# Optimization experiments

Hardware: AMD Instinct MI355X
Metric: run time of the kernel (lower is better)

## Reference

```python
import jax, jax.numpy as jnp
import numpy as np

H, D = 16, 64          # num_heads, head_dim
OUT = H * D            # out_dim = 1024
W1, W2 = 32, 32        # sliding windows
EPS_NORM = 1e-7
EPS_LN = 1e-5


def setup_inputs() -> dict:
    key = jax.random.key(0)
    ks = jax.random.split(key, 6)
    B, S, IN = 2, 2048, 1024
    x = jax.random.normal(ks[0], (B, S, IN), dtype=jnp.float32)
    scale = 0.02
    W_Q = jax.random.normal(ks[1], (IN, OUT), dtype=jnp.float32) * scale
    W_K = jax.random.normal(ks[2], (IN, OUT), dtype=jnp.float32) * scale
    W_V = jax.random.normal(ks[3], (IN, OUT), dtype=jnp.float32) * scale
    W_Kp = jax.random.normal(ks[4], (IN, OUT), dtype=jnp.float32) * scale
    W_O = jax.random.normal(ks[5], (OUT, OUT), dtype=jnp.float32) * scale
    ln_gamma = jnp.ones((OUT,), dtype=jnp.float32)
    ln_beta = jnp.zeros((OUT,), dtype=jnp.float32)
    return {"x": x, "W_Q": W_Q, "W_K": W_K, "W_V": W_V, "W_Kp": W_Kp,
            "W_O": W_O, "ln_gamma": ln_gamma, "ln_beta": ln_beta}


def _l2norm(t):
    return t / (jnp.linalg.norm(t, axis=-1, keepdims=True) + EPS_NORM)


def reference(x, W_Q, W_K, W_V, W_Kp, W_O, ln_gamma, ln_beta):
    B, S, _ = x.shape
    # projections -> (B, S, H, D)
    Q = _l2norm((x @ W_Q).reshape(B, S, H, D))
    K = _l2norm((x @ W_K).reshape(B, S, H, D))
    Kp = _l2norm((x @ W_Kp).reshape(B, S, H, D))
    V = (x @ W_V).reshape(B, S, H, D)
    # windowed keys/values (last w1/w2 positions, as in the PyTorch fallback)
    K_win = K[:, -W1:]
    Kp_win = Kp[:, -W2:]
    V_win = V[:, -W1:]
    Vp_win = V[:, -W2:]
    # triple product A_ijk = q.k.k' / sqrt(D) -> (B, S, H, w1, w2)
    A = jnp.einsum('bshd,bjhd,bkhd->bshjk', Q, K_win, Kp_win) / jnp.sqrt(jnp.float32(D))
    # causal window mask: allow j <= i + w1 - S and k <= i + w2 - S
    s_idx = jnp.arange(S)[:, None, None]
    j_idx = jnp.arange(W1)[None, :, None]
    k_idx = jnp.arange(W2)[None, None, :]
    mask = (j_idx > s_idx + (W1 - S)) | (k_idx > s_idx + (W2 - S))  # (S, w1, w2)
    neg_inf = jnp.float32(-jnp.inf)
    A = jnp.where(mask[None, :, None, :, :], neg_inf, A)
    # joint softmax over (j, k); fully-masked query rows produce zeros
    A_flat = A.reshape(B, S, H, W1 * W2)
    all_masked = jnp.all(A_flat == neg_inf, axis=-1, keepdims=True)
    A_safe = jnp.where(all_masked, 0.0, A_flat)
    P = jax.nn.softmax(A_safe, axis=-1)
    P = jnp.where(all_masked, 0.0, P).reshape(B, S, H, W1, W2)
    # value outer-product weighting (V' = V)
    Z = jnp.einsum('bshjk,bjhd,bkhd->bshd', P, V_win, Vp_win)
    out = Z.reshape(B, S, OUT) @ W_O
    out = out + x  # residual (shapes match)
    # LayerNorm
    mu = jnp.mean(out, axis=-1, keepdims=True)
    var = jnp.mean((out - mu) ** 2, axis=-1, keepdims=True)
    out = (out - mu) / jnp.sqrt(var + EPS_LN) * ln_gamma + ln_beta
    return out
```

## Files before the change

kernel.cpp:

```cpp
#include <hip/hip_runtime.h>
#include <math.h>


#define XS 68

#define YQ_OFF    0
#define YK_OFF    65536
#define YKP_OFF   131072
#define YV_OFF    196608
#define Z_OFF     262144
#define DELTA_OFF 327680
#define WS_FLOATS 393216

__global__ __launch_bounds__(256) void zero_ws(float4* __restrict__ ws) {
  ws[blockIdx.x * 256 + threadIdx.x] = make_float4(0.f, 0.f, 0.f, 0.f);
}

__global__ __launch_bounds__(256, 4) void proj_kernel(
    const float* __restrict__ x,
    const float* __restrict__ Wq, const float* __restrict__ Wk,
    const float* __restrict__ Wkp, const float* __restrict__ Wv,
    float* __restrict__ Y) {
  __shared__ float xs[64 * 65];
  const int tid = threadIdx.x;
  const int z    = blockIdx.x >> 4;
  const int col0 = (blockIdx.x & 15) * 64;
  const int k0   = blockIdx.y * 64;
  const float* __restrict__ W =
      (z == 0) ? Wq : ((z == 1) ? Wk : ((z == 2) ? Wkp : Wv));

  #pragma unroll
  for (int i = 0; i < 4; i++) {
    int e = i * 256 + tid;
    int r = e >> 4, q = e & 15;
    int b = r >> 5, t = r & 31;
    float4 v = *(const float4*)(x + ((b * 2048 + 2016 + t) * 1024 + k0 + q * 4));
    xs[(q * 4 + 0) * 65 + r] = v.x;
    xs[(q * 4 + 1) * 65 + r] = v.y;
    xs[(q * 4 + 2) * 65 + r] = v.z;
    xs[(q * 4 + 3) * 65 + r] = v.w;
  }
  __syncthreads();

  const int wave = __builtin_amdgcn_readfirstlane(tid >> 6);
  const int lane = tid & 63;
  const float* __restrict__ Wt = W + (size_t)k0 * 1024 + col0 + wave * 16;

  float acc[16];
  #pragma unroll
  for (int c = 0; c < 16; c++) acc[c] = 0.f;

  #pragma unroll 4
  for (int kk = 0; kk < 64; kk++) {
    float xv = xs[kk * 65 + lane];
    const float* __restrict__ wrow = Wt + kk * 1024;
    #pragma unroll
    for (int c = 0; c < 16; c++) acc[c] = fmaf(xv, wrow[c], acc[c]);
  }

  __syncthreads();
  #pragma unroll
  for (int c = 0; c < 16; c++) xs[lane * 65 + wave * 16 + c] = acc[c];
  __syncthreads();
  float* __restrict__ Yo = Y + z * 65536 + col0;
  #pragma unroll
  for (int i = 0; i < 16; i++) {
    int r = wave * 16 + i;
    atomicAdd(Yo + r * 1024 + lane, xs[r * 65 + lane]);
  }
}

__global__ __launch_bounds__(256) void attn_kernel(
    const float* __restrict__ Y, float* __restrict__ Zout) {
  __shared__ float Kn[32 * XS], Kp[32 * XS], Vs[32 * XS];
  __shared__ float Pt[4][32 * 33];
  __shared__ float qs[4][64];
  const int tid = threadIdx.x;
  const int wave = tid >> 6, lane = tid & 63;
  const int h = blockIdx.y, b = blockIdx.z;

  #pragma unroll
  for (int i = 0; i < 8; i++) {
    int e = i * 256 + tid;
    int row = e >> 6, d = e & 63;
    int src = (b * 32 + row) * 1024 + h * 64 + d;
    Kn[row * XS + d] = Y[YK_OFF + src];
    Kp[row * XS + d] = Y[YKP_OFF + src];
    Vs[row * XS + d] = Y[YV_OFF + src];
  }
  __syncthreads();

  for (int rr = 0; rr < 8; rr++) {
    int row = wave * 8 + rr;
    float kv = Kn[row * XS + lane];
    float s2 = kv * kv;
    #pragma unroll
    for (int off = 1; off < 64; off <<= 1) s2 += __shfl_xor(s2, off);
    Kn[row * XS + lane] = kv * (1.f / (sqrtf(s2) + 1e-7f));
    float pv = Kp[row * XS + lane];
    float p2 = pv * pv;
    #pragma unroll
    for (int off = 1; off < 64; off <<= 1) p2 += __shfl_xor(p2, off);
    Kp[row * XS + lane] = pv * (1.f / (sqrtf(p2) + 1e-7f));
  }
  __syncthreads();

  const int m = blockIdx.x * 4 + wave;
  const int r = b * 32 + m;

  float q = Y[YQ_OFF + r * 1024 + h * 64 + lane];
  float q2 = q * q;
  #pragma unroll
  for (int off = 1; off < 64; off <<= 1) q2 += __shfl_xor(q2, off);
  q *= (1.f / (sqrtf(q2) + 1e-7f));
  qs[wave][lane] = q;
  __builtin_amdgcn_wave_barrier();

  const int lj = lane >> 3, lk = lane & 7;
  float acc[4][4];
  #pragma unroll
  for (int a = 0; a < 4; a++)
    #pragma unroll
    for (int c = 0; c < 4; c++) acc[a][c] = 0.f;

  const float* qw = qs[wave];
  for (int dq = 0; dq < 16; dq++) {
    float4 q4 = *(const float4*)(qw + dq * 4);
    float4 t4[4], kp4[4];
    #pragma unroll
    for (int tj = 0; tj < 4; tj++) {
      float4 kv = *(const float4*)(Kn + (lj * 4 + tj) * XS + dq * 4);
      t4[tj].x = q4.x * kv.x; t4[tj].y = q4.y * kv.y;
      t4[tj].z = q4.z * kv.z; t4[tj].w = q4.w * kv.w;
    }
    #pragma unroll
    for (int tk = 0; tk < 4; tk++)
      kp4[tk] = *(const float4*)(Kp + (lk * 4 + tk) * XS + dq * 4);
    #pragma unroll
    for (int tj = 0; tj < 4; tj++)
      #pragma unroll
      for (int tk = 0; tk < 4; tk++)
        acc[tj][tk] += t4[tj].x * kp4[tk].x + t4[tj].y * kp4[tk].y
                     + t4[tj].z * kp4[tk].z + t4[tj].w * kp4[tk].w;
  }

  float amax = -1e30f;
  #pragma unroll
  for (int tj = 0; tj < 4; tj++)
    #pragma unroll
    for (int tk = 0; tk < 4; tk++) {
      int j = lj * 4 + tj, k = lk * 4 + tk;
      if (j <= m && k <= m) amax = fmaxf(amax, acc[tj][tk] * 0.125f);
    }
  #pragma unroll
  for (int off = 1; off < 64; off <<= 1) amax = fmaxf(amax, __shfl_xor(amax, off));

  float lsum = 0.f;
  float* ptw = Pt[wave];
  #pragma unroll
  for (int tj = 0; tj < 4; tj++)
    #pragma unroll
    for (int tk = 0; tk < 4; tk++) {
      int j = lj * 4 + tj, k = lk * 4 + tk;
      float e = 0.f;
      if (j <= m && k <= m) e = __expf(acc[tj][tk] * 0.125f - amax);
      lsum += e;
      ptw[k * 33 + j] = e;
    }
  #pragma unroll
  for (int off = 1; off < 64; off <<= 1) lsum += __shfl_xor(lsum, off);
  float inv = 1.f / lsum;
  __builtin_amdgcn_wave_barrier();

  float vreg[32];
  #pragma unroll
  for (int k = 0; k < 32; k++) vreg[k] = Vs[k * XS + lane];
  float zacc = 0.f;
  for (int k = 0; k <= m; k++) {
    float g = 0.f;
    #pragma unroll
    for (int j = 0; j < 32; j++) g += ptw[k * 33 + j] * vreg[j];
    zacc += g * vreg[k];
  }
  Zout[r * 1024 + h * 64 + lane] = zacc * inv;
}

__global__ __launch_bounds__(256, 4) void wo_kernel(
    const float* __restrict__ Zr, const float* __restrict__ Wo,
    float* __restrict__ delta) {
  __shared__ float xs[64 * 65];
  const int tid = threadIdx.x;
  const int col0 = blockIdx.x * 64;
  const int k0   = blockIdx.y * 32;

  #pragma unroll
  for (int i = 0; i < 2; i++) {
    int e = i * 256 + tid;
    int r = e >> 3, q = e & 7;
    float4 v = *(const float4*)(Zr + r * 1024 + k0 + q * 4);
    xs[(q * 4 + 0) * 65 + r] = v.x;
    xs[(q * 4 + 1) * 65 + r] = v.y;
    xs[(q * 4 + 2) * 65 + r] = v.z;
    xs[(q * 4 + 3) * 65 + r] = v.w;
  }
  __syncthreads();

  const int wave = __builtin_amdgcn_readfirstlane(tid >> 6);
  const int lane = tid & 63;
  const float* __restrict__ Wt = Wo + (size_t)k0 * 1024 + col0 + wave * 16;

  float acc[16];
  #pragma unroll
  for (int c = 0; c < 16; c++) acc[c] = 0.f;

  #pragma unroll 4
  for (int kk = 0; kk < 32; kk++) {
    float xv = xs[kk * 65 + lane];
    const float* __restrict__ wrow = Wt + kk * 1024;
    #pragma unroll
    for (int c = 0; c < 16; c++) acc[c] = fmaf(xv, wrow[c], acc[c]);
  }

  __syncthreads();
  #pragma unroll
  for (int c = 0; c < 16; c++) xs[lane * 65 + wave * 16 + c] = acc[c];
  __syncthreads();
  #pragma unroll
  for (int i = 0; i < 16; i++) {
    int r = wave * 16 + i;
    atomicAdd(delta + r * 1024 + col0 + lane, xs[r * 65 + lane]);
  }
}

__global__ __launch_bounds__(256, 4) void ln_kernel(
    const float4* __restrict__ x4, const float4* __restrict__ delta4,
    const float4* __restrict__ g4, const float4* __restrict__ b4,
    float4* __restrict__ out4) {
  const int tid = threadIdx.x;
  const int wave = tid >> 6, lane = tid & 63;
  const int row = blockIdx.x * 4 + wave;
  const int b = row >> 11, s = row & 2047;

  float4 v[4];
  #pragma unroll
  for (int i = 0; i < 4; i++) v[i] = x4[row * 256 + i * 64 + lane];
  if (s >= 2016) {
    int drow = b * 32 + (s - 2016);
    #pragma unroll
    for (int i = 0; i < 4; i++) {
      float4 d = delta4[drow * 256 + i * 64 + lane];
      v[i].x += d.x; v[i].y += d.y; v[i].z += d.z; v[i].w += d.w;
    }
  }
  float sum = 0.f, ss = 0.f;
  #pragma unroll
  for (int i = 0; i < 4; i++) {
    sum += v[i].x + v[i].y + v[i].z + v[i].w;
    ss  += v[i].x * v[i].x + v[i].y * v[i].y + v[i].z * v[i].z + v[i].w * v[i].w;
  }
  #pragma unroll
  for (int off = 1; off < 64; off <<= 1) {
    sum += __shfl_xor(sum, off);
    ss  += __shfl_xor(ss, off);
  }
  float mu   = sum * (1.f / 1024.f);
  float var  = ss * (1.f / 1024.f) - mu * mu;
  float rstd = rsqrtf(var + 1e-5f);

  #pragma unroll
  for (int i = 0; i < 4; i++) {
    float4 g = g4[i * 64 + lane];
    float4 be = b4[i * 64 + lane];
    float4 o;
    o.x = (v[i].x - mu) * rstd * g.x + be.x;
    o.y = (v[i].y - mu) * rstd * g.y + be.y;
    o.z = (v[i].z - mu) * rstd * g.z + be.z;
    o.w = (v[i].w - mu) * rstd * g.w + be.w;
    out4[row * 256 + i * 64 + lane] = o;
  }
}

extern "C" void kernel_launch(void* const* d_in, const int* in_sizes, int n_in,
                              void* d_out, int out_size, void* d_ws, size_t ws_size,
                              hipStream_t stream) {
  const float* x   = (const float*)d_in[0];
  const float* Wq  = (const float*)d_in[1];
  const float* Wk  = (const float*)d_in[2];
  const float* Wv  = (const float*)d_in[3];
  const float* Wkp = (const float*)d_in[4];
  const float* Wo  = (const float*)d_in[5];
  const float* gam = (const float*)d_in[6];
  const float* bet = (const float*)d_in[7];
  float* out = (float*)d_out;
  float* ws  = (float*)d_ws;

  hipLaunchKernelGGL(zero_ws, dim3(WS_FLOATS / 1024), dim3(256), 0, stream,
                     (float4*)ws);
  hipLaunchKernelGGL(proj_kernel, dim3(64, 16), dim3(256), 0, stream,
                     x, Wq, Wk, Wkp, Wv, ws);
  hipLaunchKernelGGL(attn_kernel, dim3(8, 16, 2), dim3(256), 0, stream,
                     ws, ws + Z_OFF);
  hipLaunchKernelGGL(wo_kernel, dim3(16, 32), dim3(256), 0, stream,
                     ws + Z_OFF, Wo, ws + DELTA_OFF);
  hipLaunchKernelGGL(ln_kernel, dim3(1024), dim3(256), 0, stream,
                     (const float4*)x, (const float4*)(ws + DELTA_OFF),
                     (const float4*)gam, (const float4*)bet, (float4*)out);
}
```

Before: 141.9 us.

## Replace atomic split-K accumulation with per-split partial buffers reduced by consumers

The projection and output-projection GEMMs now write split-K partials to separate workspace slices with plain stores instead of atomicAdd. The attention and LayerNorm kernels sum the partials when they read them, which removes the workspace-zeroing kernel and the atomic traffic. The K split changes from 64/32 to 128 with fewer blocks. Attention also gets a swizzled shared-memory layout for K and Kp and vectorised float4 P stores and loads. The cost is extra partial reads in the consumer kernels, fewer blocks in the GEMMs, and lower occupancy from the larger shared tile.

```diff
diff --git a/kernel.cpp b/kernel.cpp
--- a/kernel.cpp
+++ b/kernel.cpp
@@ -4,35 +4,34 @@
 
 #define XS 68
 
-#define YQ_OFF    0
-#define YK_OFF    65536
-#define YKP_OFF   131072
-#define YV_OFF    196608
-#define Z_OFF     262144
-#define DELTA_OFF 327680
-#define WS_FLOATS 393216
-
-__global__ __launch_bounds__(256) void zero_ws(float4* __restrict__ ws) {
-  ws[blockIdx.x * 256 + threadIdx.x] = make_float4(0.f, 0.f, 0.f, 0.f);
-}
-
-__global__ __launch_bounds__(256, 4) void proj_kernel(
+#define NSPLIT    8
+#define YPART_SZ  262144
+#define Z_OFF     (NSPLIT * YPART_SZ)
+#define DPART_OFF (Z_OFF + 65536)
+
+
+__device__ __forceinline__ int sw_idx(int row, int d) {
+  return row * 64 + ((((d >> 2) + (row >> 2)) & 15) << 2) + (d & 3);
+}
+
+__global__ __launch_bounds__(256, 2) void proj_kernel(
     const float* __restrict__ x,
     const float* __restrict__ Wq, const float* __restrict__ Wk,
     const float* __restrict__ Wkp, const float* __restrict__ Wv,
-    float* __restrict__ Y) {
-  __shared__ float xs[64 * 65];
+    float* __restrict__ ws) {
+  __shared__ float xs[128 * 65];
   const int tid = threadIdx.x;
   const int z    = blockIdx.x >> 4;
   const int col0 = (blockIdx.x & 15) * 64;
-  const int k0   = blockIdx.y * 64;
+  const int ks   = blockIdx.y;
+  const int k0   = ks * 128;
   const float* __restrict__ W =
       (z == 0) ? Wq : ((z == 1) ? Wk : ((z == 2) ? Wkp : Wv));
 
   #pragma unroll
-  for (int i = 0; i < 4; i++) {
+  for (int i = 0; i < 8; i++) {
     int e = i * 256 + tid;
-    int r = e >> 4, q = e & 15;
+    int r = e >> 5, q = e & 31;
     int b = r >> 5, t = r & 31;
     float4 v = *(const float4*)(x + ((b * 2048 + 2016 + t) * 1024 + k0 + q * 4));
     xs[(q * 4 + 0) * 65 + r] = v.x;
@@ -51,7 +50,7 @@
   for (int c = 0; c < 16; c++) acc[c] = 0.f;
 
   #pragma unroll 4
-  for (int kk = 0; kk < 64; kk++) {
+  for (int kk = 0; kk < 128; kk++) {
     float xv = xs[kk * 65 + lane];
     const float* __restrict__ wrow = Wt + kk * 1024;
     #pragma unroll
@@ -62,18 +61,19 @@
   #pragma unroll
   for (int c = 0; c < 16; c++) xs[lane * 65 + wave * 16 + c] = acc[c];
   __syncthreads();
-  float* __restrict__ Yo = Y + z * 65536 + col0;
+  float* __restrict__ Yo = ws + (size_t)ks * YPART_SZ + z * 65536 + col0;
   #pragma unroll
   for (int i = 0; i < 16; i++) {
     int r = wave * 16 + i;
-    atomicAdd(Yo + r * 1024 + lane, xs[r * 65 + lane]);
+    Yo[r * 1024 + lane] = xs[r * 65 + lane];
   }
 }
 
 __global__ __launch_bounds__(256) void attn_kernel(
-    const float* __restrict__ Y, float* __restrict__ Zout) {
-  __shared__ float Kn[32 * XS], Kp[32 * XS], Vs[32 * XS];
-  __shared__ float Pt[4][32 * 33];
+    const float* __restrict__ ws, float* __restrict__ Zout) {
+  __shared__ float Kn[32 * 64], Kp[32 * 64];
+  __shared__ float Vs[32 * XS];
+  __shared__ float Pt[4][32 * 36];
   __shared__ float qs[4][64];
   const int tid = threadIdx.x;
   const int wave = tid >> 6, lane = tid & 63;
@@ -84,31 +84,45 @@
     int e = i * 256 + tid;
     int row = e >> 6, d = e & 63;
     int src = (b * 32 + row) * 1024 + h * 64 + d;
-    Kn[row * XS + d] = Y[YK_OFF + src];
-    Kp[row * XS + d] = Y[YKP_OFF + src];
-    Vs[row * XS + d] = Y[YV_OFF + src];
+    float kn = 0.f, kp = 0.f, vv = 0.f;
+    #pragma unroll
+    for (int s = 0; s < NSPLIT; s++) {
+      const float* __restrict__ p = ws + (size_t)s * YPART_SZ + src;
+      kn += p[65536];
+      kp += p[131072];
+      vv += p[196608];
+    }
+    Kn[sw_idx(row, d)] = kn;
+    Kp[sw_idx(row, d)] = kp;
+    Vs[row * XS + d] = vv;
   }
   __syncthreads();
 
   for (int rr = 0; rr < 8; rr++) {
     int row = wave * 8 + rr;
-    float kv = Kn[row * XS + lane];
+    int a = sw_idx(row, lane);
+    float kv = Kn[a];
     float s2 = kv * kv;
     #pragma unroll
     for (int off = 1; off < 64; off <<= 1) s2 += __shfl_xor(s2, off);
-    Kn[row * XS + lane] = kv * (1.f / (sqrtf(s2) + 1e-7f));
-    float pv = Kp[row * XS + lane];
+    Kn[a] = kv * (1.f / (sqrtf(s2) + 1e-7f));
+    float pv = Kp[a];
     float p2 = pv * pv;
     #pragma unroll
     for (int off = 1; off < 64; off <<= 1) p2 += __shfl_xor(p2, off);
-    Kp[row * XS + lane] = pv * (1.f / (sqrtf(p2) + 1e-7f));
+    Kp[a] = pv * (1.f / (sqrtf(p2) + 1e-7f));
   }
   __syncthreads();
 
   const int m = blockIdx.x * 4 + wave;
   const int r = b * 32 + m;
 
-  float q = Y[YQ_OFF + r * 1024 + h * 64 + lane];
+  float q = 0.f;
+  {
+    int src = r * 1024 + h * 64 + lane;
+    #pragma unroll
+    for (int s = 0; s < NSPLIT; s++) q += ws[(size_t)s * YPART_SZ + src];
+  }
   float q2 = q * q;
   #pragma unroll
   for (int off = 1; off < 64; off <<= 1) q2 += __shfl_xor(q2, off);
@@ -126,22 +140,26 @@
   const float* qw = qs[wave];
   for (int dq = 0; dq < 16; dq++) {
     float4 q4 = *(const float4*)(qw + dq * 4);
+    const int cj = (((dq + lj) & 15) << 2);
+    const int ck = (((dq + lk) & 15) << 2);
     float4 t4[4], kp4[4];
     #pragma unroll
     for (int tj = 0; tj < 4; tj++) {
-      float4 kv = *(const float4*)(Kn + (lj * 4 + tj) * XS + dq * 4);
+      float4 kv = *(const float4*)(Kn + (lj * 4 + tj) * 64 + cj);
       t4[tj].x = q4.x * kv.x; t4[tj].y = q4.y * kv.y;
       t4[tj].z = q4.z * kv.z; t4[tj].w = q4.w * kv.w;
     }
     #pragma unroll
     for (int tk = 0; tk < 4; tk++)
-      kp4[tk] = *(const float4*)(Kp + (lk * 4 + tk) * XS + dq * 4);
-    #pragma unroll
-    for (int tj = 0; tj < 4; tj++)
+      kp4[tk] = *(const float4*)(Kp + (lk * 4 + tk) * 64 + ck);
+    #pragma unroll
+    for (int tj = 0; tj < 4; tj++) {
       #pragma unroll
-      for (int tk = 0; tk < 4; tk++)
+      for (int tk = 0; tk < 4; tk++) {
         acc[tj][tk] += t4[tj].x * kp4[tk].x + t4[tj].y * kp4[tk].y
                      + t4[tj].z * kp4[tk].z + t4[tj].w * kp4[tk].w;
+      }
+    }
   }
 
   float amax = -1e30f;
@@ -158,15 +176,20 @@
   float lsum = 0.f;
   float* ptw = Pt[wave];
   #pragma unroll
-  for (int tj = 0; tj < 4; tj++)
-    #pragma unroll
-    for (int tk = 0; tk < 4; tk++) {
-      int j = lj * 4 + tj, k = lk * 4 + tk;
-      float e = 0.f;
-      if (j <= m && k <= m) e = __expf(acc[tj][tk] * 0.125f - amax);
-      lsum += e;
-      ptw[k * 33 + j] = e;
-    }
+  for (int tk = 0; tk < 4; tk++) {
+    int k = lk * 4 + tk;
+    float4 ev;
+    float* e = (float*)&ev;
+    #pragma unroll
+    for (int tj = 0; tj < 4; tj++) {
+      int j = lj * 4 + tj;
+      float x = 0.f;
+      if (j <= m && k <= m) x = __expf(acc[tj][tk] * 0.125f - amax);
+      e[tj] = x;
+      lsum += x;
+    }
+    *(float4*)(ptw + k * 36 + lj * 4) = ev;
+  }
   #pragma unroll
   for (int off = 1; off < 64; off <<= 1) lsum += __shfl_xor(lsum, off);
   float inv = 1.f / lsum;
@@ -177,26 +200,33 @@
   for (int k = 0; k < 32; k++) vreg[k] = Vs[k * XS + lane];
   float zacc = 0.f;
   for (int k = 0; k <= m; k++) {
-    float g = 0.f;
-    #pragma unroll
-    for (int j = 0; j < 32; j++) g += ptw[k * 33 + j] * vreg[j];
-    zacc += g * vreg[k];
+    float g0 = 0.f, g1 = 0.f, g2 = 0.f, g3 = 0.f;
+    #pragma unroll
+    for (int jq = 0; jq < 8; jq++) {
+      float4 p = *(const float4*)(ptw + k * 36 + jq * 4);
+      g0 = fmaf(p.x, vreg[jq * 4 + 0], g0);
+      g1 = fmaf(p.y, vreg[jq * 4 + 1], g1);
+      g2 = fmaf(p.z, vreg[jq * 4 + 2], g2);
+      g3 = fmaf(p.w, vreg[jq * 4 + 3], g3);
+    }
+    zacc = fmaf((g0 + g1) + (g2 + g3), vreg[k], zacc);
   }
   Zout[r * 1024 + h * 64 + lane] = zacc * inv;
 }
 
-__global__ __launch_bounds__(256, 4) void wo_kernel(
+__global__ __launch_bounds__(256, 2) void wo_kernel(
     const float* __restrict__ Zr, const float* __restrict__ Wo,
-    float* __restrict__ delta) {
-  __shared__ float xs[64 * 65];
+    float* __restrict__ ws) {
+  __shared__ float xs[128 * 65];
   const int tid = threadIdx.x;
   const int col0 = blockIdx.x * 64;
-  const int k0   = blockIdx.y * 32;
-
-  #pragma unroll
-  for (int i = 0; i < 2; i++) {
+  const int ks   = blockIdx.y;
+  const int k0   = ks * 128;
+
+  #pragma unroll
+  for (int i = 0; i < 8; i++) {
     int e = i * 256 + tid;
-    int r = e >> 3, q = e & 7;
+    int r = e >> 5, q = e & 31;
     float4 v = *(const float4*)(Zr + r * 1024 + k0 + q * 4);
     xs[(q * 4 + 0) * 65 + r] = v.x;
     xs[(q * 4 + 1) * 65 + r] = v.y;
@@ -214,7 +244,7 @@
   for (int c = 0; c < 16; c++) acc[c] = 0.f;
 
   #pragma unroll 4
-  for (int kk = 0; kk < 32; kk++) {
+  for (int kk = 0; kk < 128; kk++) {
     float xv = xs[kk * 65 + lane];
     const float* __restrict__ wrow = Wt + kk * 1024;
     #pragma unroll
@@ -225,15 +255,16 @@
   #pragma unroll
   for (int c = 0; c < 16; c++) xs[lane * 65 + wave * 16 + c] = acc[c];
   __syncthreads();
+  float* __restrict__ Do = ws + (size_t)DPART_OFF + (size_t)ks * 65536 + col0;
   #pragma unroll
   for (int i = 0; i < 16; i++) {
     int r = wave * 16 + i;
-    atomicAdd(delta + r * 1024 + col0 + lane, xs[r * 65 + lane]);
+    Do[r * 1024 + lane] = xs[r * 65 + lane];
   }
 }
 
 __global__ __launch_bounds__(256, 4) void ln_kernel(
-    const float4* __restrict__ x4, const float4* __restrict__ delta4,
+    const float4* __restrict__ x4, const float4* __restrict__ dpart4,
     const float4* __restrict__ g4, const float4* __restrict__ b4,
     float4* __restrict__ out4) {
   const int tid = threadIdx.x;
@@ -248,8 +279,11 @@
     int drow = b * 32 + (s - 2016);
     #pragma unroll
     for (int i = 0; i < 4; i++) {
-      float4 d = delta4[drow * 256 + i * 64 + lane];
-      v[i].x += d.x; v[i].y += d.y; v[i].z += d.z; v[i].w += d.w;
+      #pragma unroll
+      for (int sp = 0; sp < NSPLIT; sp++) {
+        float4 d = dpart4[sp * 16384 + drow * 256 + i * 64 + lane];
+        v[i].x += d.x; v[i].y += d.y; v[i].z += d.z; v[i].w += d.w;
+      }
     }
   }
   float sum = 0.f, ss = 0.f;
@@ -294,15 +328,13 @@
   float* out = (float*)d_out;
   float* ws  = (float*)d_ws;
 
-  hipLaunchKernelGGL(zero_ws, dim3(WS_FLOATS / 1024), dim3(256), 0, stream,
-                     (float4*)ws);
-  hipLaunchKernelGGL(proj_kernel, dim3(64, 16), dim3(256), 0, stream,
+  hipLaunchKernelGGL(proj_kernel, dim3(64, 8), dim3(256), 0, stream,
                      x, Wq, Wk, Wkp, Wv, ws);
   hipLaunchKernelGGL(attn_kernel, dim3(8, 16, 2), dim3(256), 0, stream,
                      ws, ws + Z_OFF);
-  hipLaunchKernelGGL(wo_kernel, dim3(16, 32), dim3(256), 0, stream,
-                     ws + Z_OFF, Wo, ws + DELTA_OFF);
+  hipLaunchKernelGGL(wo_kernel, dim3(16, 8), dim3(256), 0, stream,
+                     ws + Z_OFF, Wo, ws);
   hipLaunchKernelGGL(ln_kernel, dim3(1024), dim3(256), 0, stream,
-                     (const float4*)x, (const float4*)(ws + DELTA_OFF),
+                     (const float4*)x, (const float4*)(ws + DPART_OFF),
                      (const float4*)gam, (const float4*)bet, (float4*)out);
 }
```

Result: slower. 148.7 us (+4.8%).
